# Kernel tuning notes

Measured on AMD Instinct MI355X. Metric: run time of the kernel, lower is better.

The kernel has to match this reference:

```python
import jax, jax.numpy as jnp
import numpy as np

COMMITMENT_COST = 0.25


def setup_inputs() -> dict:
    key = jax.random.key(0)
    k1, k2 = jax.random.split(key)
    z = jax.random.normal(k1, (64, 256, 32, 32), dtype=jnp.float32)
    codebook = jax.random.normal(k2, (512, 256), dtype=jnp.float32) * 0.02
    return {"z": z, "codebook": codebook}


def reference(z, codebook):
    B, C, H, W = z.shape
    # [B,C,H,W] -> [B*H*W, C]
    z_flat = jnp.transpose(z, (0, 2, 3, 1)).reshape(-1, C)
    # squared euclidean distances via matmul expansion (same argmin as broadcast form)
    d = (
        jnp.sum(z_flat * z_flat, axis=-1, keepdims=True)
        - 2.0 * (z_flat @ codebook.T)
        + jnp.sum(codebook * codebook, axis=-1)
    )  # [N, num_codes]
    encoding_indices = jnp.argmin(d, axis=1)  # [N]
    z_q = codebook[encoding_indices].reshape(B, H, W, C)
    z_q = jnp.transpose(z_q, (0, 3, 1, 2))  # [B,C,H,W]
    commitment_loss = COMMITMENT_COST * jnp.mean(
        (jax.lax.stop_gradient(z_q) - z) ** 2
    )
    embedding_loss = jnp.mean((z_q - jax.lax.stop_gradient(z)) ** 2)
    loss = commitment_loss + embedding_loss
    # straight-through estimator
    z_q_st = z + jax.lax.stop_gradient(z_q - z)
    return z_q_st, encoding_indices, loss
```

## Files before the change

### kernel.cpp

```cpp
#include <hip/hip_runtime.h>

#define C_DIM   256
#define K_CODES 512
#define N_POS   65536
#define OUT0_ELEMS 16777216
#define OUT1_ELEMS 65536

__global__ __launch_bounds__(256) void vq_transpose_kernel(const float* __restrict__ cb,
                                                           float* __restrict__ cbT)
{
    const int k = blockIdx.x;
    const int c = threadIdx.x;
    cbT[c * K_CODES + k] = cb[k * C_DIM + c];
}

__global__ __launch_bounds__(256) void vq_cc_kernel(const float* __restrict__ cbT,
                                                    float* __restrict__ cc)
{
    const int k = blockIdx.x * 256 + threadIdx.x;
    float s1[8], s2[8];
    #pragma unroll
    for (int j = 0; j < 8; ++j) { s1[j] = 0.f; s2[j] = 0.f; }
    for (int c8 = 0; c8 < 16; ++c8) {
        #pragma unroll
        for (int j = 0; j < 8; ++j) {
            float v = cbT[(c8 * 8 + j) * K_CODES + k];
            s1[j] = __fadd_rn(s1[j], __fmul_rn(v, v));
        }
    }
    for (int c8 = 16; c8 < 32; ++c8) {
        #pragma unroll
        for (int j = 0; j < 8; ++j) {
            float v = cbT[(c8 * 8 + j) * K_CODES + k];
            s2[j] = __fadd_rn(s2[j], __fmul_rn(v, v));
        }
    }
    float b1 = __fadd_rn(__fadd_rn(__fadd_rn(s1[0], s1[1]), __fadd_rn(s1[2], s1[3])),
                         __fadd_rn(__fadd_rn(s1[4], s1[5]), __fadd_rn(s1[6], s1[7])));
    float b2 = __fadd_rn(__fadd_rn(__fadd_rn(s2[0], s2[1]), __fadd_rn(s2[2], s2[3])),
                         __fadd_rn(__fadd_rn(s2[4], s2[5]), __fadd_rn(s2[6], s2[7])));
    cc[k] = __fadd_rn(b1, b2);
}

__global__ __launch_bounds__(256) void vq_zz_kernel(const float* __restrict__ z,
                                                    float* __restrict__ zz)
{
    const int pos = blockIdx.x * 256 + threadIdx.x;
    const float* zp = z + ((size_t)(pos >> 10) << 18) + (pos & 1023);
    float s1[8], s2[8];
    #pragma unroll
    for (int j = 0; j < 8; ++j) { s1[j] = 0.f; s2[j] = 0.f; }
    for (int c8 = 0; c8 < 16; ++c8) {
        #pragma unroll
        for (int j = 0; j < 8; ++j) {
            float v = zp[(size_t)(c8 * 8 + j) << 10];
            s1[j] = __fadd_rn(s1[j], __fmul_rn(v, v));
        }
    }
    for (int c8 = 16; c8 < 32; ++c8) {
        #pragma unroll
        for (int j = 0; j < 8; ++j) {
            float v = zp[(size_t)(c8 * 8 + j) << 10];
            s2[j] = __fadd_rn(s2[j], __fmul_rn(v, v));
        }
    }
    float b1 = __fadd_rn(__fadd_rn(__fadd_rn(s1[0], s1[1]), __fadd_rn(s1[2], s1[3])),
                         __fadd_rn(__fadd_rn(s1[4], s1[5]), __fadd_rn(s1[6], s1[7])));
    float b2 = __fadd_rn(__fadd_rn(__fadd_rn(s2[0], s2[1]), __fadd_rn(s2[2], s2[3])),
                         __fadd_rn(__fadd_rn(s2[4], s2[5]), __fadd_rn(s2[6], s2[7])));
    zz[pos] = __fadd_rn(b1, b2);
}

__global__ __launch_bounds__(256) void vq_main_kernel(
    const float* __restrict__ z, const float* __restrict__ cbT,
    const float* __restrict__ ccv, const float* __restrict__ zzbuf,
    float* __restrict__ bd, int* __restrict__ bc)
{
    const int blk   = blockIdx.x;
    const int cg    = blk & 3;
    const int chunk = blk >> 2;
    const int b     = chunk >> 4;
    const int hw0   = (chunk & 15) << 6;
    const int tid   = threadIdx.x;
    const int lane  = tid & 63;
    const int w     = tid >> 6;
    const int pos   = (b << 10) + hw0 + lane;

    const float* zp = z + ((size_t)b << 18) + hw0 + lane;
    const int cb0   = __builtin_amdgcn_readfirstlane((cg << 7) + (w << 5));
    const float* cbbase = cbT + cb0;

    float acc[32];
    #pragma unroll
    for (int k = 0; k < 32; ++k) acc[k] = 0.f;

    for (int c = 0; c < C_DIM; ++c) {
        const float zv = zp[(size_t)c << 10];
        const float* cbrow = cbbase + (c << 9);
        #pragma unroll
        for (int k = 0; k < 32; ++k)
            acc[k] = __builtin_fmaf(zv, cbrow[k], acc[k]);
    }

    const float zzv = zzbuf[pos];
    const float* ccp = ccv + cb0;
    float bestd = 3.4e38f;
    int   bestc = cb0;
    #pragma unroll
    for (int k = 0; k < 32; ++k) {
        float d = __fadd_rn(__fsub_rn(zzv, __fmul_rn(2.0f, acc[k])), ccp[k]);
        if (d < bestd) { bestd = d; bestc = cb0 + k; }
    }

    __shared__ float sdm[4][64];
    __shared__ int   sco[4][64];
    sdm[w][lane] = bestd;
    sco[w][lane] = bestc;
    __syncthreads();

    if (w == 0) {
        float bdv = sdm[0][lane];
        int   bcv = sco[0][lane];
        #pragma unroll
        for (int ww = 1; ww < 4; ++ww) {
            float d2 = sdm[ww][lane];
            int   c2 = sco[ww][lane];
            if (d2 < bdv || (d2 == bdv && c2 < bcv)) { bdv = d2; bcv = c2; }
        }
        bd[(cg << 16) + pos] = bdv;
        bc[(cg << 16) + pos] = bcv;
    }
}

__global__ __launch_bounds__(256) void vq_combine_kernel(
    const float* __restrict__ bd, const int* __restrict__ bc,
    int* __restrict__ idx, float* __restrict__ out1, float* __restrict__ partials)
{
    const int t   = threadIdx.x;
    const int pos = blockIdx.x * 256 + t;
    float bdv = bd[pos];
    int   bcv = bc[pos];
    #pragma unroll
    for (int g = 1; g < 4; ++g) {
        float d2 = bd[(g << 16) + pos];
        int   c2 = bc[(g << 16) + pos];
        if (d2 < bdv || (d2 == bdv && c2 < bcv)) { bdv = d2; bcv = c2; }
    }
    idx[pos]  = bcv;
    out1[pos] = (float)bcv;

    __shared__ float s[256];
    s[t] = bdv;
    __syncthreads();
    for (int off = 128; off > 0; off >>= 1) {
        if (t < off) s[t] += s[t + off];
        __syncthreads();
    }
    if (t == 0) partials[blockIdx.x] = s[0];
}

__global__ __launch_bounds__(256) void vq_gather_kernel(
    const float* __restrict__ cb, const int* __restrict__ idx,
    float* __restrict__ out0)
{
    const int blk = blockIdx.x;
    const int b   = blk >> 4;
    const int hw0 = (blk & 15) << 6;
    const int lane = threadIdx.x & 63;
    const int w    = threadIdx.x >> 6;

    __shared__ int sidx[64];
    if (threadIdx.x < 64) sidx[threadIdx.x] = idx[(blk << 6) + threadIdx.x];
    __syncthreads();

    const int code = sidx[lane];
    const float4* crow4 = reinterpret_cast<const float4*>(cb + ((size_t)code << 8) + (w << 6));
    float* ob = out0 + ((size_t)b << 18) + ((size_t)(w * 64) << 10) + hw0 + lane;
    #pragma unroll 4
    for (int j4 = 0; j4 < 16; ++j4) {
        float4 v = crow4[j4];
        ob[(size_t)(j4 * 4 + 0) << 10] = v.x;
        ob[(size_t)(j4 * 4 + 1) << 10] = v.y;
        ob[(size_t)(j4 * 4 + 2) << 10] = v.z;
        ob[(size_t)(j4 * 4 + 3) << 10] = v.w;
    }
}

__global__ __launch_bounds__(256) void vq_finalize_kernel(
    const float* __restrict__ partials, float* __restrict__ out2)
{
    __shared__ float s[256];
    const int t = threadIdx.x;
    s[t] = partials[t];
    __syncthreads();
    for (int off = 128; off > 0; off >>= 1) {
        if (t < off) s[t] += s[t + off];
        __syncthreads();
    }
    if (t == 0)
        out2[0] = 1.25f * (s[0] * (1.0f / 16777216.0f));
}

extern "C" void kernel_launch(void* const* d_in, const int* in_sizes, int n_in,
                              void* d_out, int out_size, void* d_ws, size_t ws_size,
                              hipStream_t stream)
{
    const float* z  = (const float*)d_in[0];
    const float* cb = (const float*)d_in[1];

    float* out0 = (float*)d_out;
    float* out1 = out0 + OUT0_ELEMS;
    float* out2 = out0 + OUT0_ELEMS + OUT1_ELEMS;

    float* bd = out0;
    int*   bc = (int*)(out0 + 4 * N_POS);
    float* zz = out0 + 8 * N_POS;

    float* wsf      = (float*)d_ws;
    float* partials = wsf;
    float* ccv      = wsf + 256;
    float* cbT      = wsf + 1024;
    int*   idx      = (int*)(wsf + 1024 + C_DIM * K_CODES);

    hipLaunchKernelGGL(vq_transpose_kernel, dim3(512),  dim3(256), 0, stream, cb, cbT);
    hipLaunchKernelGGL(vq_cc_kernel,        dim3(2),    dim3(256), 0, stream, cbT, ccv);
    hipLaunchKernelGGL(vq_zz_kernel,        dim3(256),  dim3(256), 0, stream, z, zz);
    hipLaunchKernelGGL(vq_main_kernel,      dim3(4096), dim3(256), 0, stream,
                       z, cbT, ccv, zz, bd, bc);
    hipLaunchKernelGGL(vq_combine_kernel,   dim3(256),  dim3(256), 0, stream,
                       bd, bc, idx, out1, partials);
    hipLaunchKernelGGL(vq_gather_kernel,    dim3(1024), dim3(256), 0, stream, cb, idx, out0);
    hipLaunchKernelGGL(vq_finalize_kernel,  dim3(1),    dim3(256), 0, stream, partials, out2);
}
```

Baseline: 241.3 us.

## Register-block four positions per thread in the distance kernel to reuse codebook loads

```diff
diff --git a/kernel.cpp b/kernel.cpp
--- a/kernel.cpp
+++ b/kernel.cpp
@@ -71,7 +71,7 @@
     zz[pos] = __fadd_rn(b1, b2);
 }
 
-__global__ __launch_bounds__(256) void vq_main_kernel(
+__global__ __launch_bounds__(256, 3) void vq_main_kernel(
     const float* __restrict__ z, const float* __restrict__ cbT,
     const float* __restrict__ ccv, const float* __restrict__ zzbuf,
     float* __restrict__ bd, int* __restrict__ bc)
@@ -79,56 +79,73 @@
     const int blk   = blockIdx.x;
     const int cg    = blk & 3;
     const int chunk = blk >> 2;
-    const int b     = chunk >> 4;
-    const int hw0   = (chunk & 15) << 6;
+    const int b     = chunk >> 2;
+    const int hw0   = (chunk & 3) << 8;
     const int tid   = threadIdx.x;
     const int lane  = tid & 63;
     const int w     = tid >> 6;
-    const int pos   = (b << 10) + hw0 + lane;
 
     const float* zp = z + ((size_t)b << 18) + hw0 + lane;
     const int cb0   = __builtin_amdgcn_readfirstlane((cg << 7) + (w << 5));
     const float* cbbase = cbT + cb0;
 
-    float acc[32];
-    #pragma unroll
-    for (int k = 0; k < 32; ++k) acc[k] = 0.f;
+    float acc[4][32];
+    #pragma unroll
+    for (int p = 0; p < 4; ++p)
+        #pragma unroll
+        for (int k = 0; k < 32; ++k) acc[p][k] = 0.f;
 
     for (int c = 0; c < C_DIM; ++c) {
-        const float zv = zp[(size_t)c << 10];
+        const float* zc = zp + ((size_t)c << 10);
+        const float zv0 = zc[0];
+        const float zv1 = zc[64];
+        const float zv2 = zc[128];
+        const float zv3 = zc[192];
         const float* cbrow = cbbase + (c << 9);
         #pragma unroll
-        for (int k = 0; k < 32; ++k)
-            acc[k] = __builtin_fmaf(zv, cbrow[k], acc[k]);
-    }
-
-    const float zzv = zzbuf[pos];
+        for (int k = 0; k < 32; ++k) {
+            const float cv = cbrow[k];
+            acc[0][k] = __builtin_fmaf(zv0, cv, acc[0][k]);
+            acc[1][k] = __builtin_fmaf(zv1, cv, acc[1][k]);
+            acc[2][k] = __builtin_fmaf(zv2, cv, acc[2][k]);
+            acc[3][k] = __builtin_fmaf(zv3, cv, acc[3][k]);
+        }
+    }
+
+    __shared__ float sdm[4][4][64];
+    __shared__ int   sco[4][4][64];
+
     const float* ccp = ccv + cb0;
-    float bestd = 3.4e38f;
-    int   bestc = cb0;
-    #pragma unroll
-    for (int k = 0; k < 32; ++k) {
-        float d = __fadd_rn(__fsub_rn(zzv, __fmul_rn(2.0f, acc[k])), ccp[k]);
-        if (d < bestd) { bestd = d; bestc = cb0 + k; }
-    }
-
-    __shared__ float sdm[4][64];
-    __shared__ int   sco[4][64];
-    sdm[w][lane] = bestd;
-    sco[w][lane] = bestc;
+    const int posb = (b << 10) + hw0 + lane;
+    #pragma unroll
+    for (int p = 0; p < 4; ++p) {
+        const float zzv = zzbuf[posb + p * 64];
+        float bestd = 3.4e38f;
+        int   bestc = cb0;
+        #pragma unroll
+        for (int k = 0; k < 32; ++k) {
+            float d = __fadd_rn(__fsub_rn(zzv, __fmul_rn(2.0f, acc[p][k])), ccp[k]);
+            if (d < bestd) { bestd = d; bestc = cb0 + k; }
+        }
+        sdm[w][p][lane] = bestd;
+        sco[w][p][lane] = bestc;
+    }
     __syncthreads();
 
     if (w == 0) {
-        float bdv = sdm[0][lane];
-        int   bcv = sco[0][lane];
-        #pragma unroll
-        for (int ww = 1; ww < 4; ++ww) {
-            float d2 = sdm[ww][lane];
-            int   c2 = sco[ww][lane];
-            if (d2 < bdv || (d2 == bdv && c2 < bcv)) { bdv = d2; bcv = c2; }
-        }
-        bd[(cg << 16) + pos] = bdv;
-        bc[(cg << 16) + pos] = bcv;
+        #pragma unroll
+        for (int p = 0; p < 4; ++p) {
+            float bdv = sdm[0][p][lane];
+            int   bcv = sco[0][p][lane];
+            #pragma unroll
+            for (int ww = 1; ww < 4; ++ww) {
+                float d2 = sdm[ww][p][lane];
+                int   c2 = sco[ww][p][lane];
+                if (d2 < bdv || (d2 == bdv && c2 < bcv)) { bdv = d2; bcv = c2; }
+            }
+            bd[(cg << 16) + posb + p * 64] = bdv;
+            bc[(cg << 16) + posb + p * 64] = bcv;
+        }
     }
 }
 
@@ -225,7 +242,7 @@
     hipLaunchKernelGGL(vq_transpose_kernel, dim3(512),  dim3(256), 0, stream, cb, cbT);
     hipLaunchKernelGGL(vq_cc_kernel,        dim3(2),    dim3(256), 0, stream, cbT, ccv);
     hipLaunchKernelGGL(vq_zz_kernel,        dim3(256),  dim3(256), 0, stream, z, zz);
-    hipLaunchKernelGGL(vq_main_kernel,      dim3(4096), dim3(256), 0, stream,
+    hipLaunchKernelGGL(vq_main_kernel,      dim3(1024), dim3(256), 0, stream,
                        z, cbT, ccv, zz, bd, bc);
     hipLaunchKernelGGL(vq_combine_kernel,   dim3(256),  dim3(256), 0, stream,
                        bd, bc, idx, out1, partials);
```

Result: slower. 279.0 us (+15.6%).
